# Performance work log

Measured on AMD Instinct MI355X. Metric: run time of the kernel, lower is better.

The kernel has to match this reference:

```python
import jax, jax.numpy as jnp
import numpy as np

N_EMBD = 1024
HEAD_SIZE = 128


def setup_inputs() -> dict:
    key = jax.random.key(0)
    k_x, k_w, k_cov, k_b = jax.random.split(key, 4)
    x = jax.random.normal(k_x, (16384, 2, N_EMBD), dtype=jnp.float32)
    # values_proj: nn.Linear(n_embd, head_size, bias=False) -> weight [head_size, n_embd]
    W = jax.random.normal(k_w, (HEAD_SIZE, N_EMBD), dtype=jnp.float32) * (N_EMBD ** -0.5)
    cov = jax.random.normal(k_cov, (HEAD_SIZE, HEAD_SIZE), dtype=jnp.float32) * (HEAD_SIZE ** -0.5)
    bias = jax.random.normal(k_b, (HEAD_SIZE,), dtype=jnp.float32)
    return {"x": x, "W": W, "cov": cov, "bias": bias}


def reference(x, W, cov, bias):
    # x: [B, 2, E]; W: [H, E]; cov: [H, H]; bias: [H]
    values = jnp.einsum('be,he->bh', x[:, 0, :], W)  # [B, H]
    mask = jnp.einsum('be,he->bh', x[:, 1, :], W)    # [B, H]
    # diag_embed(mask) @ cov == mask[:, :, None] * cov  -> [B, H, H]
    coeffs = jax.nn.softmax(mask[:, :, None] * cov[None, :, :], axis=-1)
    # values.unsqueeze(1) @ coeffs + bias, then [:, 0, :]
    out = jnp.einsum('bh,bhk->bk', values, coeffs) + bias
    return out
```

## Files before the change

kernel.cpp:

```cpp
#include <hip/hip_runtime.h>

#define LOG2E 1.4426950408889634f

typedef __attribute__((ext_vector_type(8))) short frag_ab;
typedef __attribute__((ext_vector_type(4))) float frag_cd;

__device__ inline short f2bf(float f) {
    union { float f; unsigned u; } v; v.f = f;
    unsigned r = v.u + 0x7fffu + ((v.u >> 16) & 1u);
    return (short)(r >> 16);
}

template<int CTRL>
__device__ inline float dpp_ror_add(float x) {
    int t = __builtin_amdgcn_update_dpp(0, __builtin_bit_cast(int, x), CTRL, 0xf, 0xf, false);
    return x + __builtin_bit_cast(float, t);
}

#define GLD_TO_LDS(gp, lp)                                                              \
    __builtin_amdgcn_global_load_lds((const __attribute__((address_space(1))) void*)(gp), \
                                     (__attribute__((address_space(3))) void*)(lp), 16, 0, 0)

#define PACK_AF(af, p0, p1)                                                   \
    af[0] = f2bf(p0.x); af[1] = f2bf(p0.y); af[2] = f2bf(p0.z); af[3] = f2bf(p0.w); \
    af[4] = f2bf(p1.x); af[5] = f2bf(p1.y); af[6] = f2bf(p1.z); af[7] = f2bf(p1.w);

__global__ __launch_bounds__(256) void prep_kernel(const float* __restrict__ W,
                                                   short* __restrict__ wbf) {
    int g = blockIdx.x * 256 + threadIdx.x;
    int h = g >> 7;
    int k0 = (g & 127) << 3;
    const float* src = W + h * 1024 + k0;
    float4 w0 = *(const float4*)src;
    float4 w1 = *(const float4*)(src + 4);
    frag_ab af;
    PACK_AF(af, w0, w1);
    int c = k0 >> 6, s = (k0 >> 5) & 1, kg = (k0 >> 3) & 3;
    int nt = h >> 4, m = h & 15, lane = kg * 16 + m;
    int dst = (((c * 8 + nt) * 2 + s) * 64 + lane) * 8;
    *(frag_ab*)(wbf + dst) = af;
}

__global__ __launch_bounds__(256, 2) void proj_kernel(const float* __restrict__ x,
                                                      const short* __restrict__ wbf,
                                                      float* __restrict__ vm) {
    __shared__ __align__(16) char smem[32768];

    const int tid = threadIdx.x;
    const int lane = tid & 63, wave = tid >> 6;
    const int m = lane & 15, kg = lane >> 4;
    const long rowbase = (long)blockIdx.x * 64 + wave * 16;
    const float* xrow = x + (rowbase + m) * 1024 + kg * 8;

    frag_cd acc[8];
#pragma unroll
    for (int nt = 0; nt < 8; ++nt) acc[nt] = (frag_cd){0.f, 0.f, 0.f, 0.f};

    {
        const char* wc = (const char*)wbf;
        GLD_TO_LDS(wc + tid * 16,         smem + tid * 16);
        GLD_TO_LDS(wc + 4096 + tid * 16,  smem + 4096 + tid * 16);
        GLD_TO_LDS(wc + 8192 + tid * 16,  smem + 8192 + tid * 16);
        GLD_TO_LDS(wc + 12288 + tid * 16, smem + 12288 + tid * 16);
    }
    float4 a0 = *(const float4*)(xrow);
    float4 a1 = *(const float4*)(xrow + 4);
    float4 a2 = *(const float4*)(xrow + 32);
    float4 a3 = *(const float4*)(xrow + 36);
    __syncthreads();

    int cb = 0;
    for (int c = 0; c < 16; ++c) {
        float4 n0, n1, n2, n3;
        if (c < 15) {
            const char* wc = (const char*)wbf + (c + 1) * 16384;
            char* bd = smem + (cb ^ 1) * 16384;
            GLD_TO_LDS(wc + tid * 16,         bd + tid * 16);
            GLD_TO_LDS(wc + 4096 + tid * 16,  bd + 4096 + tid * 16);
            GLD_TO_LDS(wc + 8192 + tid * 16,  bd + 8192 + tid * 16);
            GLD_TO_LDS(wc + 12288 + tid * 16, bd + 12288 + tid * 16);
            const float* xn = xrow + (c + 1) * 64;
            n0 = *(const float4*)(xn);
            n1 = *(const float4*)(xn + 4);
            n2 = *(const float4*)(xn + 32);
            n3 = *(const float4*)(xn + 36);
        }
        frag_ab af0, af1;
        PACK_AF(af0, a0, a1);
        PACK_AF(af1, a2, a3);

        const char* bs = smem + cb * 16384;
#pragma unroll
        for (int nt = 0; nt < 8; ++nt) {
            frag_ab bf0 = *(const frag_ab*)(bs + (nt * 2 + 0) * 1024 + lane * 16);
            acc[nt] = __builtin_amdgcn_mfma_f32_16x16x32_bf16(af0, bf0, acc[nt], 0, 0, 0);
            frag_ab bf1 = *(const frag_ab*)(bs + (nt * 2 + 1) * 1024 + lane * 16);
            acc[nt] = __builtin_amdgcn_mfma_f32_16x16x32_bf16(af1, bf1, acc[nt], 0, 0, 0);
        }
        if (c < 15) { a0 = n0; a1 = n1; a2 = n2; a3 = n3; }
        __syncthreads();
        cb ^= 1;
    }

#pragma unroll
    for (int nt = 0; nt < 8; ++nt)
#pragma unroll
        for (int r = 0; r < 4; ++r) {
            long row = rowbase + kg * 4 + r;
            vm[row * 128 + nt * 16 + m] = acc[nt][r];
        }
}

__global__ __launch_bounds__(512, 4) void combine_kernel(const float* __restrict__ vm,
                                                         const float* __restrict__ cov,
                                                         const float* __restrict__ bias,
                                                         float* __restrict__ out) {
    __shared__ float obuf[4][32][132];

    const int t = threadIdx.x;
    const int i = t >> 4;
    const int j = t & 15;
    const float bias_own = bias[t & 127];

    float covreg[4][8];
#pragma unroll
    for (int hh = 0; hh < 4; ++hh) {
        const float* cr = cov + (long)(i * 4 + hh) * 128 + j * 8;
        float4 c0 = *(const float4*)cr;
        float4 c1 = *(const float4*)(cr + 4);
        covreg[hh][0] = LOG2E * c0.x; covreg[hh][1] = LOG2E * c0.y;
        covreg[hh][2] = LOG2E * c0.z; covreg[hh][3] = LOG2E * c0.w;
        covreg[hh][4] = LOG2E * c1.x; covreg[hh][5] = LOG2E * c1.y;
        covreg[hh][6] = LOG2E * c1.z; covreg[hh][7] = LOG2E * c1.w;
    }

    const long b0 = (long)blockIdx.x * 8;
    for (int rr = 0; rr < 2; ++rr) {
#pragma unroll
        for (int sb = 0; sb < 4; ++sb) {
            const long b = b0 + rr * 4 + sb;
            float4 v4 = *(const float4*)(vm + (2 * b) * 128 + i * 4);
            float4 m4 = *(const float4*)(vm + (2 * b + 1) * 128 + i * 4);
            float vh[4] = {v4.x, v4.y, v4.z, v4.w};
            float mh[4] = {m4.x, m4.y, m4.z, m4.w};
            float op[8] = {0.f, 0.f, 0.f, 0.f, 0.f, 0.f, 0.f, 0.f};
#pragma unroll
            for (int hh = 0; hh < 4; ++hh) {
                float mv = mh[hh];
                float p[8];
#pragma unroll
                for (int kk = 0; kk < 8; ++kk)
                    p[kk] = __builtin_amdgcn_exp2f(mv * covreg[hh][kk]);
                float s0 = p[0] + p[1], s1 = p[2] + p[3];
                float s2 = p[4] + p[5], s3 = p[6] + p[7];
                float lsum = (s0 + s1) + (s2 + s3);
                lsum = dpp_ror_add<0x121>(lsum);
                lsum = dpp_ror_add<0x122>(lsum);
                lsum = dpp_ror_add<0x124>(lsum);
                lsum = dpp_ror_add<0x128>(lsum);
                float w = vh[hh] * __builtin_amdgcn_rcpf(lsum);
#pragma unroll
                for (int kk = 0; kk < 8; ++kk) op[kk] = fmaf(w, p[kk], op[kk]);
            }
            *(float4*)&obuf[sb][i][j * 8]     = make_float4(op[0], op[1], op[2], op[3]);
            *(float4*)&obuf[sb][i][j * 8 + 4] = make_float4(op[4], op[5], op[6], op[7]);
        }
        __syncthreads();
        {
            const int k  = t & 127;
            const int sb = t >> 7;
            float o = bias_own;
#pragma unroll
            for (int ii = 0; ii < 32; ++ii) o += obuf[sb][ii][k];
            out[(b0 + rr * 4 + sb) * 128 + k] = o;
        }
        __syncthreads();
    }
}

extern "C" void kernel_launch(void* const* d_in, const int* in_sizes, int n_in,
                              void* d_out, int out_size, void* d_ws, size_t ws_size,
                              hipStream_t stream) {
    const float* x    = (const float*)d_in[0];
    const float* W    = (const float*)d_in[1];
    const float* cov  = (const float*)d_in[2];
    const float* bias = (const float*)d_in[3];
    float* out = (float*)d_out;

    const int B = in_sizes[0] / (2 * 1024);

    short* wbf = (short*)d_ws;
    float* vm  = (float*)(wbf + 128 * 1024);

    prep_kernel<<<64, 256, 0, stream>>>(W, wbf);
    proj_kernel<<<(2 * B) / 64, 256, 0, stream>>>(x, wbf, vm);
    combine_kernel<<<B / 8, 512, 0, stream>>>(vm, cov, bias, out);
}
```

Baseline: 255.3 us.

## Read bf16 weight fragments directly from global and shrink combine LDS buffer

The projection kernel drops the LDS double-buffered weight staging and its per-chunk barriers. Each wave now loads its bf16 weight fragments straight from global memory, where they are expected to hit in cache, and the occupancy hint rises to 4 blocks. The combine kernel halves its shared output buffer by handling 2 batches per sub-round instead of 4, raising the occupancy hint to 6. The trade-offs are redundant global/L2 weight traffic per wave in place of shared-memory reuse, and more barriers in combine with half the threads idle during the reduction.

```diff
diff --git a/kernel.cpp b/kernel.cpp
--- a/kernel.cpp
+++ b/kernel.cpp
@@ -16,10 +16,6 @@
     int t = __builtin_amdgcn_update_dpp(0, __builtin_bit_cast(int, x), CTRL, 0xf, 0xf, false);
     return x + __builtin_bit_cast(float, t);
 }
-
-#define GLD_TO_LDS(gp, lp)                                                              \
-    __builtin_amdgcn_global_load_lds((const __attribute__((address_space(1))) void*)(gp), \
-                                     (__attribute__((address_space(3))) void*)(lp), 16, 0, 0)
 
 #define PACK_AF(af, p0, p1)                                                   \
     af[0] = f2bf(p0.x); af[1] = f2bf(p0.y); af[2] = f2bf(p0.z); af[3] = f2bf(p0.w); \
@@ -41,44 +37,28 @@
     *(frag_ab*)(wbf + dst) = af;
 }
 
-__global__ __launch_bounds__(256, 2) void proj_kernel(const float* __restrict__ x,
+__global__ __launch_bounds__(256, 4) void proj_kernel(const float* __restrict__ x,
                                                       const short* __restrict__ wbf,
                                                       float* __restrict__ vm) {
-    __shared__ __align__(16) char smem[32768];
-
     const int tid = threadIdx.x;
     const int lane = tid & 63, wave = tid >> 6;
     const int m = lane & 15, kg = lane >> 4;
     const long rowbase = (long)blockIdx.x * 64 + wave * 16;
     const float* xrow = x + (rowbase + m) * 1024 + kg * 8;
+    const frag_ab* wb = (const frag_ab*)wbf + lane;
 
     frag_cd acc[8];
 #pragma unroll
     for (int nt = 0; nt < 8; ++nt) acc[nt] = (frag_cd){0.f, 0.f, 0.f, 0.f};
 
-    {
-        const char* wc = (const char*)wbf;
-        GLD_TO_LDS(wc + tid * 16,         smem + tid * 16);
-        GLD_TO_LDS(wc + 4096 + tid * 16,  smem + 4096 + tid * 16);
-        GLD_TO_LDS(wc + 8192 + tid * 16,  smem + 8192 + tid * 16);
-        GLD_TO_LDS(wc + 12288 + tid * 16, smem + 12288 + tid * 16);
-    }
     float4 a0 = *(const float4*)(xrow);
     float4 a1 = *(const float4*)(xrow + 4);
     float4 a2 = *(const float4*)(xrow + 32);
     float4 a3 = *(const float4*)(xrow + 36);
-    __syncthreads();
 
-    int cb = 0;
     for (int c = 0; c < 16; ++c) {
         float4 n0, n1, n2, n3;
         if (c < 15) {
-            const char* wc = (const char*)wbf + (c + 1) * 16384;
-            char* bd = smem + (cb ^ 1) * 16384;
-            GLD_TO_LDS(wc + tid * 16,         bd + tid * 16);
-            GLD_TO_LDS(wc + 4096 + tid * 16,  bd + 4096 + tid * 16);
-            GLD_TO_LDS(wc + 8192 + tid * 16,  bd + 8192 + tid * 16);
-            GLD_TO_LDS(wc + 12288 + tid * 16, bd + 12288 + tid * 16);
             const float* xn = xrow + (c + 1) * 64;
             n0 = *(const float4*)(xn);
             n1 = *(const float4*)(xn + 4);
@@ -89,17 +69,15 @@
         PACK_AF(af0, a0, a1);
         PACK_AF(af1, a2, a3);
 
-        const char* bs = smem + cb * 16384;
+        const frag_ab* bp = wb + (size_t)c * 1024;
 #pragma unroll
         for (int nt = 0; nt < 8; ++nt) {
-            frag_ab bf0 = *(const frag_ab*)(bs + (nt * 2 + 0) * 1024 + lane * 16);
+            frag_ab bf0 = bp[(nt * 2 + 0) * 64];
             acc[nt] = __builtin_amdgcn_mfma_f32_16x16x32_bf16(af0, bf0, acc[nt], 0, 0, 0);
-            frag_ab bf1 = *(const frag_ab*)(bs + (nt * 2 + 1) * 1024 + lane * 16);
+            frag_ab bf1 = bp[(nt * 2 + 1) * 64];
             acc[nt] = __builtin_amdgcn_mfma_f32_16x16x32_bf16(af1, bf1, acc[nt], 0, 0, 0);
         }
         if (c < 15) { a0 = n0; a1 = n1; a2 = n2; a3 = n3; }
-        __syncthreads();
-        cb ^= 1;
     }
 
 #pragma unroll
@@ -111,11 +89,11 @@
         }
 }
 
-__global__ __launch_bounds__(512, 4) void combine_kernel(const float* __restrict__ vm,
+__global__ __launch_bounds__(512, 6) void combine_kernel(const float* __restrict__ vm,
                                                          const float* __restrict__ cov,
                                                          const float* __restrict__ bias,
                                                          float* __restrict__ out) {
-    __shared__ float obuf[4][32][132];
+    __shared__ float obuf[2][32][132];
 
     const int t = threadIdx.x;
     const int i = t >> 4;
@@ -135,10 +113,10 @@
     }
 
     const long b0 = (long)blockIdx.x * 8;
-    for (int rr = 0; rr < 2; ++rr) {
+    for (int rr = 0; rr < 4; ++rr) {
 #pragma unroll
-        for (int sb = 0; sb < 4; ++sb) {
-            const long b = b0 + rr * 4 + sb;
+        for (int sb = 0; sb < 2; ++sb) {
+            const long b = b0 + rr * 2 + sb;
             float4 v4 = *(const float4*)(vm + (2 * b) * 128 + i * 4);
             float4 m4 = *(const float4*)(vm + (2 * b + 1) * 128 + i * 4);
             float vh[4] = {v4.x, v4.y, v4.z, v4.w};
@@ -166,13 +144,13 @@
             *(float4*)&obuf[sb][i][j * 8 + 4] = make_float4(op[4], op[5], op[6], op[7]);
         }
         __syncthreads();
-        {
+        if (t < 256) {
             const int k  = t & 127;
             const int sb = t >> 7;
             float o = bias_own;
 #pragma unroll
             for (int ii = 0; ii < 32; ++ii) o += obuf[sb][ii][k];
-            out[(b0 + rr * 4 + sb) * 128 + k] = o;
+            out[(b0 + rr * 2 + sb) * 128 + k] = o;
         }
         __syncthreads();
     }
```

Result: slower. 310.3 us (+21.5%).
